# Kernel optimization log

Measured on AMD Instinct MI355X. Metric: run time of the kernel, lower is better.

Reference implementation:

```python
import jax, jax.numpy as jnp
import numpy as np

B, F, Q, E = 256, 128, 4096, 128
TAU = 0.2
P_DROP = 0.5
NUM_SAMPLES = 128  # hardcoded in forward: compute_scores(..., num_samples=128)
NUM_POS = 1
EASY_UB = 0.5
HARD_LB = 0.5


def setup_inputs() -> dict:
    k = jax.random.key(0)
    ks = jax.random.split(k, 8)
    query = jax.random.normal(ks[0], (B, F), jnp.float32)
    key = jax.random.normal(ks[1], (B, F), jnp.float32)
    teacher = jax.random.normal(ks[2], (B, F), jnp.float32)
    negatives = jax.random.normal(ks[3], (F, Q), jnp.float32)
    # random_maskout masks: rand <= p -> zero out
    mask_t = jax.random.uniform(ks[4], (E, B, F)) <= P_DROP
    mask_n = jax.random.uniform(ks[5], (E, F, Q)) <= P_DROP
    # compute_scores sampling mask: rand <= num_samples/Q
    score_mask = jax.random.uniform(ks[6], (E, B, Q)) <= (NUM_SAMPLES / Q)
    # bootstrap over batch dim: for each (e,q) column, sample B row indices with replacement
    idx = jax.random.randint(ks[7], (E, Q, B), 0, B)
    boot = jnp.zeros((E, Q, B), bool).at[
        jnp.arange(E)[:, None, None], jnp.arange(Q)[None, :, None], idx
    ].set(True)
    boot_mask = jnp.transpose(boot, (0, 2, 1))  # (E,B,Q)
    return dict(query=query, key=key, teacher=teacher, negatives=negatives,
                mask_t=mask_t, mask_n=mask_n, score_mask=score_mask, boot_mask=boot_mask)


def _masked_softmax(x, mask, axis):
    # matches torch masked_fill(~mask, -inf) + softmax; masked entries -> 0 prob
    z = jnp.where(mask, x, -jnp.inf)
    m = jnp.max(z, axis=axis, keepdims=True)
    m = jnp.where(jnp.isfinite(m), m, 0.0)  # guard fully-masked slices
    e = jnp.where(mask, jnp.exp(z - m), 0.0)
    return e / jnp.maximum(e.sum(axis=axis, keepdims=True), 1e-30)


def _l2norm(x, axis):
    n = jnp.sqrt(jnp.sum(x * x, axis=axis, keepdims=True))
    return x / jnp.maximum(n, 1e-12)


def reference(query, key, teacher, negatives, mask_t, mask_n, score_mask, boot_mask):
    negatives = jax.lax.stop_gradient(negatives)  # negatives.detach().clone()
    logits_pos = jnp.sum(query * key, axis=1, keepdims=True)      # (B,1)
    logits_neg = query @ negatives                                 # (B,Q)
    logits = jnp.concatenate([logits_pos, logits_neg], axis=1) / TAU
    moco_loss = -jax.nn.log_softmax(logits, axis=1)[:, 0].mean()   # CE with target 0

    # ---- teacher similarities (torch.no_grad) ----
    t = _l2norm(jnp.where(mask_t, 0.0, teacher[None, :, :]), 2)    # (E,B,F)
    n = _l2norm(jnp.where(mask_n, 0.0, negatives[None, :, :]), 1)  # (E,F,Q)
    sim = jax.lax.stop_gradient(jnp.einsum('ebf,efq->ebq', t, n) / TAU)

    # ---- scores: masked softmax over Q, masked mean over E ----
    probs = _masked_softmax(sim, score_mask, axis=2)               # (E,B,Q)
    cnt_e = jnp.maximum(score_mask.sum(axis=0).astype(sim.dtype), 1.0)
    scores = probs.sum(axis=0) / cnt_e                             # (B,Q)

    # ---- uncertainty: masked entropy over batch dim ----
    p = _masked_softmax(sim, boot_mask, axis=1) + 1e-7             # (E,B,Q)
    ent = -(p * jnp.log(p))
    cnt_b = jnp.maximum(boot_mask.sum(axis=1).astype(sim.dtype), 1.0)  # (E,Q)
    uncertainty = (ent.sum(axis=1) / cnt_b).mean(axis=0, keepdims=True)  # (1,Q)

    log_sm_neg = jax.nn.log_softmax(logits[:, 1:], axis=1)         # (B,Q)

    def _pos_loss(pos_mask_row):
        pm = jnp.broadcast_to(pos_mask_row, (B, Q))
        s = jnp.where(pm, scores, -jnp.inf)
        _, idx = jax.lax.top_k(s, NUM_POS)                         # (B,k)
        loss = -jnp.take_along_axis(log_sm_neg, idx, axis=1).mean(axis=1).mean()
        mask = jnp.zeros((B, Q), bool).at[jnp.arange(B)[:, None], idx].set(True)
        return loss, mask

    ub = jnp.quantile(uncertainty, EASY_UB, axis=1)                # (1,)
    easy_loss, easy_mask = _pos_loss(uncertainty <= ub)
    lb = jnp.quantile(uncertainty, HARD_LB, axis=1)
    hard_loss, hard_mask = _pos_loss(uncertainty >= lb)

    return moco_loss, logits, easy_loss, easy_mask, hard_loss, hard_mask
```

## Files before the change

### kernel.cpp

```cpp
#include <hip/hip_runtime.h>
#include <cmath>

typedef unsigned char u8;
typedef unsigned short u16;
typedef unsigned int u32;
typedef __attribute__((ext_vector_type(8))) short s8v;
typedef __attribute__((ext_vector_type(4))) float f32x4;

#define B 256
#define F 128
#define Q 4096
#define E 128
#define QW 128
#define INV_TAU 5.0f
#define CAP 256

#define W_SCORES 0u
#define W_CNT    1048576u
#define W_UNC    2097152u
#define W_NLSE   2101248u
#define W_MOCO   2101504u
#define W_EASY   2101760u
#define W_HARD   2102016u
#define W_UB     2102272u
#define W_INVN   2102528u
#define W_AF     2626816u
#define W_PB     4723968u
#define W_PS     8918272u
#define W_PN     13112576u
#define W_CNTB   15209728u
#define W_ENT    15242496u

#define O_MOCO   0u
#define O_LOGITS 1u
#define O_ELOSS  1048833u
#define O_EMASK  1048834u
#define O_HLOSS  2097410u
#define O_HMASK  2097411u

static __device__ __forceinline__ u16 f2bf(float x) {
    unsigned int u = __builtin_bit_cast(unsigned int, x);
    unsigned int r = (u + 0x7FFFu + ((u >> 16) & 1u)) >> 16;
    return (u16)r;
}

__global__ void k_zero(float4* __restrict__ p) {
    p[(size_t)blockIdx.x * 256 + threadIdx.x] = make_float4(0.f, 0.f, 0.f, 0.f);
}
__global__ void k_zeroi(int* __restrict__ p) {
    p[(size_t)blockIdx.x * 256 + threadIdx.x] = 0;
}

__global__ void __launch_bounds__(256) k_pack(const u8* __restrict__ in,
                                              u32* __restrict__ out, int Rin) {
    __shared__ u32 lds[64 * 133];
    int t = threadIdx.x;
    int r0 = blockIdx.x * 64;
    int q0 = blockIdx.y * 512;
    int qw0 = q0 >> 5;
    #pragma unroll
    for (int i = 0; i < 8; i++) {
        int w = i * 256 + t;
        int row = w >> 5, c = w & 31;
        uint4 v = *(const uint4*)&in[(size_t)(r0 + row) * Q + q0 + c * 16];
        int base = row * 133 + c * 4;
        lds[base] = v.x; lds[base + 1] = v.y; lds[base + 2] = v.z; lds[base + 3] = v.w;
    }
    __syncthreads();
    int e = r0 / Rin, rr = r0 % Rin;
    #pragma unroll
    for (int k = 0; k < 4; k++) {
        int qw = (t >> 6) + k * 4;
        int r = t & 63;
        u32 w = 0;
        #pragma unroll
        for (int j = 0; j < 8; j++) {
            u32 u = lds[r * 133 + qw * 8 + j];
            w |= ((u & 1u) | ((u >> 7) & 2u) | ((u >> 14) & 4u) | ((u >> 21) & 8u)) << (j * 4);
        }
        out[((size_t)e * QW + qw0 + qw) * Rin + rr + r] = w;
    }
}

__global__ void k_afrag(const float* __restrict__ teacher, const u8* __restrict__ mask_t,
                        u16* __restrict__ af) {
    int eb = blockIdx.x;
    int e  = eb >> 8;
    int b  = eb & (B - 1);
    int f  = threadIdx.x;
    float v = mask_t[(size_t)eb * F + f] ? 0.f : teacher[b * F + f];
    float ss = v * v;
    #pragma unroll
    for (int o = 32; o > 0; o >>= 1) ss += __shfl_down(ss, o);
    __shared__ float s2[2];
    if ((threadIdx.x & 63) == 0) s2[threadIdx.x >> 6] = ss;
    __syncthreads();
    float d = fmaxf(sqrtf(s2[0] + s2[1]), 1e-12f);
    float t = v / d;
    int bg = b >> 4, m = b & 15;
    int kb = f >> 5, quad = (f >> 3) & 3, j = f & 7;
    int lane = quad * 16 + m;
    af[((((size_t)e * 16 + bg) * 4 + kb) * 64 + lane) * 8 + j] = f2bf(t);
}

__global__ void __launch_bounds__(256) k_invn(const float* __restrict__ neg,
                                              const u32* __restrict__ pn,
                                              float* __restrict__ invn) {
    __shared__ u32 lds[32 * 128];
    int e = blockIdx.x, t = threadIdx.x;
    int qblk = blockIdx.y;
    size_t base = ((size_t)e * QW + qblk * 32) * F;
    #pragma unroll
    for (int k = 0; k < 16; k++) lds[t + 256 * k] = pn[base + t + 256 * k];
    __syncthreads();
    int q0 = qblk * 1024 + t * 4;
    int qwl = (t * 4) >> 5;
    int sh = (t * 4) & 31;
    float s0 = 0.f, s1 = 0.f, s2 = 0.f, s3 = 0.f;
    #pragma unroll 4
    for (int f = 0; f < F; f++) {
        float4 v = *(const float4*)&neg[(size_t)f * Q + q0];
        u32 w = lds[qwl * 128 + f] >> sh;
        if (!(w & 1u)) s0 = fmaf(v.x, v.x, s0);
        if (!(w & 2u)) s1 = fmaf(v.y, v.y, s1);
        if (!(w & 4u)) s2 = fmaf(v.z, v.z, s2);
        if (!(w & 8u)) s3 = fmaf(v.w, v.w, s3);
    }
    float4 r;
    r.x = INV_TAU / fmaxf(sqrtf(s0), 1e-12f);
    r.y = INV_TAU / fmaxf(sqrtf(s1), 1e-12f);
    r.z = INV_TAU / fmaxf(sqrtf(s2), 1e-12f);
    r.w = INV_TAU / fmaxf(sqrtf(s3), 1e-12f);
    *(float4*)&invn[(size_t)e * Q + q0] = r;
}

__global__ void __launch_bounds__(256) k_fused(
        const u16* __restrict__ af, const float* __restrict__ neg,
        const u32* __restrict__ pn, const float* __restrict__ invn,
        const u32* __restrict__ pb, const u32* __restrict__ ps,
        float* __restrict__ unc, uint2* __restrict__ ent_buf,
        int* __restrict__ cnt_buf, int e0) {
    __shared__ u16 bfrag[2][4][64 * 8];
    __shared__ __align__(16) u32 bword[256];
    __shared__ __align__(16) u32 sword[256];
    __shared__ int sbase[256];
    __shared__ float mstat[4][32], sstat[4][32], cstat[4][32], estat[4][32];
    __shared__ float carr[32];

    int qb = blockIdx.x;
    int el = blockIdx.y, e = e0 + el;
    int t = threadIdx.x;
    int q0 = qb * 32;

    bword[t] = pb[((size_t)e * QW + qb) * B + t];
    sword[t] = ps[((size_t)e * QW + qb) * B + t];

    #pragma unroll
    for (int s = 0; s < 2; s++) {
        int slot = t + 256 * s;
        int qg = slot >> 8;
        int r = slot & 255;
        int kb = r >> 6, lane2 = r & 63;
        int q = q0 + qg * 16 + (lane2 & 15);
        int fb = kb * 32 + (lane2 >> 4) * 8;
        float iv = invn[e * Q + q];
        u16 tmp[8];
        #pragma unroll
        for (int j = 0; j < 8; j++) {
            u32 bit = (pn[((size_t)e * QW + qb) * F + fb + j] >> (q & 31)) & 1u;
            float v = bit ? 0.f : neg[(size_t)(fb + j) * Q + q] * iv;
            tmp[j] = f2bf(v);
        }
        *(s8v*)&bfrag[qg][kb][lane2 * 8] = *(const s8v*)tmp;
    }
    __syncthreads();

    int wave = t >> 6, lane = t & 63;
    int colb = lane & 15, quad = lane >> 4;
    f32x4 acc[4][2];
    #pragma unroll
    for (int bgi = 0; bgi < 4; bgi++) {
        int bg = wave * 4 + bgi;
        s8v a[4];
        #pragma unroll
        for (int kb = 0; kb < 4; kb++)
            a[kb] = *(const s8v*)&af[((((size_t)e * 16 + bg) * 4 + kb) * 64 + lane) * 8];
        #pragma unroll
        for (int qg = 0; qg < 2; qg++) {
            f32x4 c4 = {0.f, 0.f, 0.f, 0.f};
            #pragma unroll
            for (int kb = 0; kb < 4; kb++) {
                s8v bv = *(const s8v*)&bfrag[qg][kb][lane * 8];
                c4 = __builtin_amdgcn_mfma_f32_16x16x32_bf16(a[kb], bv, c4, 0, 0, 0);
            }
            acc[bgi][qg] = c4;
        }
    }

    u32 bwr[4][4];
    #pragma unroll
    for (int bgi = 0; bgi < 4; bgi++) {
        int b0 = (wave * 4 + bgi) * 16 + quad * 4;
        uint4 v = *(const uint4*)&bword[b0];
        bwr[bgi][0] = v.x; bwr[bgi][1] = v.y; bwr[bgi][2] = v.z; bwr[bgi][3] = v.w;
    }

    float mloc[2] = {-INFINITY, -INFINITY};
    #pragma unroll
    for (int bgi = 0; bgi < 4; bgi++)
        #pragma unroll
        for (int r = 0; r < 4; r++)
            #pragma unroll
            for (int qg = 0; qg < 2; qg++)
                if ((bwr[bgi][r] >> (qg * 16 + colb)) & 1u)
                    mloc[qg] = fmaxf(mloc[qg], acc[bgi][qg][r]);
    #pragma unroll
    for (int qg = 0; qg < 2; qg++) {
        mloc[qg] = fmaxf(mloc[qg], __shfl_xor(mloc[qg], 16));
        mloc[qg] = fmaxf(mloc[qg], __shfl_xor(mloc[qg], 32));
    }
    if (quad == 0) { mstat[wave][colb] = mloc[0]; mstat[wave][16 + colb] = mloc[1]; }
    __syncthreads();
    float Mg[2];
    #pragma unroll
    for (int qg = 0; qg < 2; qg++) {
        int col = qg * 16 + colb;
        float M = fmaxf(fmaxf(mstat[0][col], mstat[1][col]),
                        fmaxf(mstat[2][col], mstat[3][col]));
        Mg[qg] = (M == -INFINITY) ? 0.f : M;
    }

    float ex[4][2][4];
    float sloc[2] = {0.f, 0.f}, cloc[2] = {0.f, 0.f};
    #pragma unroll
    for (int bgi = 0; bgi < 4; bgi++)
        #pragma unroll
        for (int r = 0; r < 4; r++)
            #pragma unroll
            for (int qg = 0; qg < 2; qg++) {
                bool mk = (bwr[bgi][r] >> (qg * 16 + colb)) & 1u;
                float v = mk ? __expf(acc[bgi][qg][r] - Mg[qg]) : 0.f;
                ex[bgi][qg][r] = v;
                sloc[qg] += v;
                cloc[qg] += mk ? 1.f : 0.f;
            }
    #pragma unroll
    for (int qg = 0; qg < 2; qg++) {
        sloc[qg] += __shfl_xor(sloc[qg], 16); sloc[qg] += __shfl_xor(sloc[qg], 32);
        cloc[qg] += __shfl_xor(cloc[qg], 16); cloc[qg] += __shfl_xor(cloc[qg], 32);
    }
    if (quad == 0) {
        sstat[wave][colb] = sloc[0]; sstat[wave][16 + colb] = sloc[1];
        cstat[wave][colb] = cloc[0]; cstat[wave][16 + colb] = cloc[1];
    }
    __syncthreads();
    float invS[2];
    #pragma unroll
    for (int qg = 0; qg < 2; qg++) {
        int col = qg * 16 + colb;
        float S = sstat[0][col] + sstat[1][col] + sstat[2][col] + sstat[3][col];
        invS[qg] = 1.f / fmaxf(S, 1e-30f);
        if (wave == 0 && quad == 0)
            carr[col] = cstat[0][col] + cstat[1][col] + cstat[2][col] + cstat[3][col];
    }

    const float P0 = 1e-7f;
    const float C0 = 1.61180954e-6f;
    float eloc[2] = {0.f, 0.f};
    #pragma unroll
    for (int bgi = 0; bgi < 4; bgi++)
        #pragma unroll
        for (int r = 0; r < 4; r++)
            #pragma unroll
            for (int qg = 0; qg < 2; qg++) {
                if ((bwr[bgi][r] >> (qg * 16 + colb)) & 1u) {
                    float p = ex[bgi][qg][r] * invS[qg] + P0;
                    eloc[qg] -= p * __logf(p);
                } else {
                    eloc[qg] += C0;
                }
            }
    #pragma unroll
    for (int qg = 0; qg < 2; qg++) {
        eloc[qg] += __shfl_xor(eloc[qg], 16); eloc[qg] += __shfl_xor(eloc[qg], 32);
    }
    if (quad == 0) { estat[wave][colb] = eloc[0]; estat[wave][16 + colb] = eloc[1]; }

    {
        u32 sw = sword[t];
        int n = __popc(sw);
        int base = 0;
        if (n) base = atomicAdd(&cnt_buf[el * B + t], n);
        sbase[t] = base;
    }
    __syncthreads();

    if (t < 32) {
        float tot = estat[0][t] + estat[1][t] + estat[2][t] + estat[3][t];
        atomicAdd(&unc[q0 + t], tot / fmaxf(carr[t], 1.f));
    }

    #pragma unroll
    for (int bgi = 0; bgi < 4; bgi++) {
        int b0 = (wave * 4 + bgi) * 16 + quad * 4;
        uint4 sv = *(const uint4*)&sword[b0];
        u32 svr[4] = {sv.x, sv.y, sv.z, sv.w};
        #pragma unroll
        for (int r = 0; r < 4; r++)
            #pragma unroll
            for (int qg = 0; qg < 2; qg++) {
                int c = qg * 16 + colb;
                u32 w = svr[r];
                if ((w >> c) & 1u) {
                    int pos = sbase[b0 + r] + __popc(w & ((1u << c) - 1u));
                    if (pos < CAP) {
                        uint2 en;
                        en.x = (unsigned)(q0 + c);
                        en.y = __builtin_bit_cast(unsigned, acc[bgi][qg][r]);
                        ent_buf[((size_t)(el * B + b0 + r)) * CAP + pos] = en;
                    }
                }
            }
    }
}

__global__ void __launch_bounds__(256) k_scores(
        const uint2* __restrict__ ent_buf, const int* __restrict__ cnt_buf,
        float* __restrict__ sacc, float* __restrict__ cacc, int ecnt) {
    __shared__ float srow[Q];
    __shared__ float crow[Q];
    int b = blockIdx.x, t = threadIdx.x;
    #pragma unroll
    for (int j = 0; j < 16; j++) { srow[t + 256 * j] = 0.f; crow[t + 256 * j] = 0.f; }
    __syncthreads();
    int wave = t >> 6, lane = t & 63;
    for (int el = wave; el < ecnt; el += 4) {
        int c = cnt_buf[el * B + b];
        if (c > CAP) c = CAP;
        if (c == 0) continue;
        const uint2* p = ent_buf + (size_t)(el * B + b) * CAP;
        uint2 ev[4]; int ne = 0;
        float m = -INFINITY;
        for (int i = lane; i < c; i += 64) {
            ev[ne] = p[i];
            m = fmaxf(m, __builtin_bit_cast(float, ev[ne].y));
            ne++;
        }
        #pragma unroll
        for (int off = 32; off > 0; off >>= 1) m = fmaxf(m, __shfl_xor(m, off));
        float s = 0.f; float exv[4];
        for (int k = 0; k < ne; k++) {
            exv[k] = __expf(__builtin_bit_cast(float, ev[k].y) - m);
            s += exv[k];
        }
        #pragma unroll
        for (int off = 32; off > 0; off >>= 1) s += __shfl_xor(s, off);
        float iS = 1.f / fmaxf(s, 1e-30f);
        for (int k = 0; k < ne; k++) {
            atomicAdd(&srow[ev[k].x], exv[k] * iS);
            atomicAdd(&crow[ev[k].x], 1.f);
        }
    }
    __syncthreads();
    #pragma unroll
    for (int j = 0; j < 16; j++) {
        int q = t + 256 * j;
        sacc[(size_t)b * Q + q] += srow[q];
        cacc[(size_t)b * Q + q] += crow[q];
    }
}

__global__ void k_finscores(float* __restrict__ sacc, const float* __restrict__ cacc) {
    int idx = blockIdx.x * 256 + threadIdx.x;
    sacc[idx] = sacc[idx] / fmaxf(cacc[idx], 1.f);
}

__global__ void k_logits(const float* __restrict__ query, const float* __restrict__ key,
                         const float* __restrict__ neg, float* __restrict__ out) {
    __shared__ float qrow[F];
    __shared__ float red[256];
    int b = blockIdx.x, t = threadIdx.x;
    float pp = 0.f;
    if (t < F) { float qv = query[b * F + t]; qrow[t] = qv; pp = qv * key[b * F + t]; }
    red[t] = pp;
    __syncthreads();
    for (int s = 128; s > 0; s >>= 1) { if (t < s) red[t] += red[t + s]; __syncthreads(); }
    float pos = red[0];
    float4 acc[4];
    #pragma unroll
    for (int j = 0; j < 4; j++) acc[j] = make_float4(0.f, 0.f, 0.f, 0.f);
    for (int f = 0; f < F; f++) {
        float a = qrow[f];
        const float* np_ = neg + (size_t)f * Q + t * 4;
        #pragma unroll
        for (int j = 0; j < 4; j++) {
            float4 v = *(const float4*)&np_[1024 * j];
            acc[j].x = fmaf(a, v.x, acc[j].x);
            acc[j].y = fmaf(a, v.y, acc[j].y);
            acc[j].z = fmaf(a, v.z, acc[j].z);
            acc[j].w = fmaf(a, v.w, acc[j].w);
        }
    }
    float* row = out + O_LOGITS + (size_t)b * (Q + 1);
    #pragma unroll
    for (int j = 0; j < 4; j++) {
        int q = t * 4 + 1024 * j;
        row[1 + q]     = acc[j].x * INV_TAU;
        row[1 + q + 1] = acc[j].y * INV_TAU;
        row[1 + q + 2] = acc[j].z * INV_TAU;
        row[1 + q + 3] = acc[j].w * INV_TAU;
    }
    if (t == 0) row[0] = pos * INV_TAU;
}

__global__ void k_rowstats(const float* __restrict__ out, float* __restrict__ moco_part,
                           float* __restrict__ nlse) {
    __shared__ float red[256];
    int b = blockIdx.x, t = threadIdx.x;
    const float* row = out + O_LOGITS + (size_t)b * (Q + 1);
    float m = -INFINITY, mn = -INFINITY;
    for (int j = 0; j < 17; j++) {
        int i = t + 256 * j;
        if (i < Q + 1) { float zz = row[i]; m = fmaxf(m, zz); if (i >= 1) mn = fmaxf(mn, zz); }
    }
    red[t] = m; __syncthreads();
    for (int s = 128; s > 0; s >>= 1) { if (t < s) red[t] = fmaxf(red[t], red[t + s]); __syncthreads(); }
    float M = red[0]; __syncthreads();
    red[t] = mn; __syncthreads();
    for (int s = 128; s > 0; s >>= 1) { if (t < s) red[t] = fmaxf(red[t], red[t + s]); __syncthreads(); }
    float Mn = red[0]; __syncthreads();
    float s1 = 0.f, s2 = 0.f;
    for (int j = 0; j < 17; j++) {
        int i = t + 256 * j;
        if (i < Q + 1) { float zz = row[i]; s1 += expf(zz - M); if (i >= 1) s2 += expf(zz - Mn); }
    }
    red[t] = s1; __syncthreads();
    for (int s = 128; s > 0; s >>= 1) { if (t < s) red[t] += red[t + s]; __syncthreads(); }
    float S = red[0]; __syncthreads();
    red[t] = s2; __syncthreads();
    for (int s = 128; s > 0; s >>= 1) { if (t < s) red[t] += red[t + s]; __syncthreads(); }
    float Sn = red[0];
    if (t == 0) { moco_part[b] = M + logf(S) - row[0]; nlse[b] = Mn + logf(Sn); }
}

__global__ void k_median(float* __restrict__ unc, float* __restrict__ ubp) {
    __shared__ float sd[4096];
    int t = threadIdx.x;
    #pragma unroll
    for (int j = 0; j < 4; j++) {
        int q = t + 1024 * j;
        float u = unc[q] * (1.f / 128.f);
        unc[q] = u; sd[q] = u;
    }
    __syncthreads();
    for (int k = 2; k <= 4096; k <<= 1) {
        for (int j = k >> 1; j > 0; j >>= 1) {
            #pragma unroll
            for (int base = 0; base < 4; base++) {
                int i = t + 1024 * base;
                int ixj = i ^ j;
                if (ixj > i) {
                    bool up = ((i & k) == 0);
                    float x = sd[i], y = sd[ixj];
                    if ((x > y) == up) { sd[i] = y; sd[ixj] = x; }
                }
            }
            __syncthreads();
        }
    }
    if (t == 0) { float a = sd[2047], b2 = sd[2048]; ubp[0] = a + 0.5f * (b2 - a); }
}

__global__ void k_select(float* __restrict__ out, const float* __restrict__ scores,
                         const float* __restrict__ unc, const float* __restrict__ ubp,
                         const float* __restrict__ nlse, float* __restrict__ easy_part,
                         float* __restrict__ hard_part) {
    __shared__ float rv[256];
    __shared__ int ri[256];
    __shared__ int bshare;
    int b = blockIdx.x, mode = blockIdx.y, t = threadIdx.x;
    float ub = ubp[0];
    float bv = -INFINITY; int bidx = Q;
    #pragma unroll
    for (int j = 0; j < 16; j++) {
        int q = t + 256 * j;
        float u = unc[q];
        bool ok = (mode == 0) ? (u <= ub) : (u >= ub);
        if (ok) {
            float v = scores[(size_t)b * Q + q];
            if (v > bv || (v == bv && q < bidx)) { bv = v; bidx = q; }
        }
    }
    rv[t] = bv; ri[t] = bidx; __syncthreads();
    for (int s = 128; s > 0; s >>= 1) {
        if (t < s) {
            float v2 = rv[t + s]; int i2 = ri[t + s];
            if (v2 > rv[t] || (v2 == rv[t] && i2 < ri[t])) { rv[t] = v2; ri[t] = i2; }
        }
        __syncthreads();
    }
    if (t == 0) {
        int best = ri[0]; bshare = best;
        float zz = out[O_LOGITS + (size_t)b * (Q + 1) + 1 + best];
        float loss = nlse[b] - zz;
        (mode == 0 ? easy_part : hard_part)[b] = loss;
    }
    __syncthreads();
    int best = bshare;
    float* mrow = out + (mode == 0 ? O_EMASK : O_HMASK) + (size_t)b * Q;
    #pragma unroll
    for (int j = 0; j < 16; j++) { int q = t + 256 * j; mrow[q] = (q == best) ? 1.f : 0.f; }
}

__global__ void k_scalars(const float* __restrict__ moco, const float* __restrict__ easyp,
                          const float* __restrict__ hardp, float* __restrict__ out) {
    __shared__ float red[256];
    int t = threadIdx.x;
    red[t] = moco[t]; __syncthreads();
    for (int s = 128; s > 0; s >>= 1) { if (t < s) red[t] += red[t + s]; __syncthreads(); }
    if (t == 0) out[O_MOCO] = red[0] / 256.f;
    __syncthreads();
    red[t] = easyp[t]; __syncthreads();
    for (int s = 128; s > 0; s >>= 1) { if (t < s) red[t] += red[t + s]; __syncthreads(); }
    if (t == 0) out[O_ELOSS] = red[0] / 256.f;
    __syncthreads();
    red[t] = hardp[t]; __syncthreads();
    for (int s = 128; s > 0; s >>= 1) { if (t < s) red[t] += red[t + s]; __syncthreads(); }
    if (t == 0) out[O_HLOSS] = red[0] / 256.f;
}

extern "C" void kernel_launch(void* const* d_in, const int* in_sizes, int n_in,
                              void* d_out, int out_size, void* d_ws, size_t ws_size,
                              hipStream_t stream) {
    const float* query   = (const float*)d_in[0];
    const float* key     = (const float*)d_in[1];
    const float* teacher = (const float*)d_in[2];
    const float* neg     = (const float*)d_in[3];
    const u8* mask_t     = (const u8*)d_in[4];
    const u8* mask_n     = (const u8*)d_in[5];
    const u8* score_mask = (const u8*)d_in[6];
    const u8* boot_mask  = (const u8*)d_in[7];
    float* out = (float*)d_out;
    float* ws  = (float*)d_ws;

    long ws_floats = (long)(ws_size / 4);
    int Ec = (int)((ws_floats - (long)W_ENT) / (long)(B * CAP * 2));
    if (Ec > E) Ec = E;
    if (Ec < 1) Ec = 1;

    u16* af = (u16*)(ws + W_AF);
    u32* pb = (u32*)(ws + W_PB);
    u32* ps = (u32*)(ws + W_PS);
    u32* pn = (u32*)(ws + W_PN);
    int* cnt_buf = (int*)(ws + W_CNTB);
    uint2* ent_buf = (uint2*)(ws + W_ENT);

    k_zero<<<2052, 256, 0, stream>>>((float4*)(ws + W_SCORES));
    k_pack<<<dim3((E * B) / 64, Q / 512), 256, 0, stream>>>(boot_mask, pb, B);
    k_pack<<<dim3((E * B) / 64, Q / 512), 256, 0, stream>>>(score_mask, ps, B);
    k_pack<<<dim3((E * F) / 64, Q / 512), 256, 0, stream>>>(mask_n, pn, F);
    k_afrag<<<E * B, 128, 0, stream>>>(teacher, mask_t, af);
    k_invn<<<dim3(E, 4), 256, 0, stream>>>(neg, pn, ws + W_INVN);
    k_logits<<<B, 256, 0, stream>>>(query, key, neg, out);
    k_rowstats<<<B, 256, 0, stream>>>(out, ws + W_MOCO, ws + W_NLSE);

    for (int e0 = 0; e0 < E; e0 += Ec) {
        int ecnt = (E - e0 < Ec) ? (E - e0) : Ec;
        k_zeroi<<<ecnt, 256, 0, stream>>>(cnt_buf);
        k_fused<<<dim3(QW, ecnt), 256, 0, stream>>>(
            af, neg, pn, ws + W_INVN, pb, ps, ws + W_UNC, ent_buf, cnt_buf, e0);
        k_scores<<<B, 256, 0, stream>>>(ent_buf, cnt_buf, ws + W_SCORES, ws + W_CNT, ecnt);
    }

    k_finscores<<<(B * Q) / 256, 256, 0, stream>>>(ws + W_SCORES, ws + W_CNT);
    k_median<<<1, 1024, 0, stream>>>(ws + W_UNC, ws + W_UB);
    k_select<<<dim3(B, 2), 256, 0, stream>>>(out, ws + W_SCORES, ws + W_UNC, ws + W_UB,
                                             ws + W_NLSE, ws + W_EASY, ws + W_HARD);
    k_scalars<<<1, 256, 0, stream>>>(ws + W_MOCO, ws + W_EASY, ws + W_HARD, out);
}
```

Measured before the change: 1.429 ms.

## Widen fused tile to 64 columns, drop max-subtraction, split logits kernel

The fused similarity/entropy kernel now processes 64 Q columns per block instead of 32, staging the mask words and inverse norms in shared memory so each A fragment load feeds twice as many MFMAs. The max-reduction pass and one barrier are removed from both the fused softmax and the score softmax by exponentiating raw values, which relies on the cosine-similarity/tau values being bounded. The entropy pass recomputes exp instead of keeping an exp array in registers. The logits kernel is split across four Q segments to raise parallelism.

```diff
diff --git a/kernel.cpp b/kernel.cpp
--- a/kernel.cpp
+++ b/kernel.cpp
@@ -140,35 +140,48 @@
         const u32* __restrict__ pb, const u32* __restrict__ ps,
         float* __restrict__ unc, uint2* __restrict__ ent_buf,
         int* __restrict__ cnt_buf, int e0) {
-    __shared__ u16 bfrag[2][4][64 * 8];
-    __shared__ __align__(16) u32 bword[256];
-    __shared__ __align__(16) u32 sword[256];
+    __shared__ u16 bfrag[4][4][512];
+    __shared__ u32 bw[2][256], sw[2][256];
+    __shared__ u32 pnl[2][128];
+    __shared__ float invl[64];
+    __shared__ float sstat[4][64], cstat[4][64], estat[4][64];
+    __shared__ float carr[64];
     __shared__ int sbase[256];
-    __shared__ float mstat[4][32], sstat[4][32], cstat[4][32], estat[4][32];
-    __shared__ float carr[32];
 
     int qb = blockIdx.x;
     int el = blockIdx.y, e = e0 + el;
     int t = threadIdx.x;
-    int q0 = qb * 32;
-
-    bword[t] = pb[((size_t)e * QW + qb) * B + t];
-    sword[t] = ps[((size_t)e * QW + qb) * B + t];
-
-    #pragma unroll
-    for (int s = 0; s < 2; s++) {
+    int q0 = qb * 64;
+    int qw0 = qb * 2;
+
+    bw[0][t] = pb[((size_t)e * QW + qw0) * B + t];
+    bw[1][t] = pb[((size_t)e * QW + qw0 + 1) * B + t];
+    sw[0][t] = ps[((size_t)e * QW + qw0) * B + t];
+    sw[1][t] = ps[((size_t)e * QW + qw0 + 1) * B + t];
+    if (t < 128) {
+        pnl[0][t] = pn[((size_t)e * QW + qw0) * F + t];
+        pnl[1][t] = pn[((size_t)e * QW + qw0 + 1) * F + t];
+    } else if (t < 192) {
+        invl[t - 128] = invn[(size_t)e * Q + q0 + (t - 128)];
+    }
+    __syncthreads();
+
+    #pragma unroll
+    for (int s = 0; s < 4; s++) {
         int slot = t + 256 * s;
         int qg = slot >> 8;
         int r = slot & 255;
         int kb = r >> 6, lane2 = r & 63;
-        int q = q0 + qg * 16 + (lane2 & 15);
+        int ql = qg * 16 + (lane2 & 15);
         int fb = kb * 32 + (lane2 >> 4) * 8;
-        float iv = invn[e * Q + q];
+        float iv = invl[ql];
+        const u32* pw = pnl[ql >> 5];
+        int sh = ql & 31;
         u16 tmp[8];
         #pragma unroll
         for (int j = 0; j < 8; j++) {
-            u32 bit = (pn[((size_t)e * QW + qb) * F + fb + j] >> (q & 31)) & 1u;
-            float v = bit ? 0.f : neg[(size_t)(fb + j) * Q + q] * iv;
+            u32 bit = (pw[fb + j] >> sh) & 1u;
+            float v = bit ? 0.f : neg[(size_t)(fb + j) * Q + q0 + ql] * iv;
             tmp[j] = f2bf(v);
         }
         *(s8v*)&bfrag[qg][kb][lane2 * 8] = *(const s8v*)tmp;
@@ -177,7 +190,7 @@
 
     int wave = t >> 6, lane = t & 63;
     int colb = lane & 15, quad = lane >> 4;
-    f32x4 acc[4][2];
+    f32x4 acc[4][4];
     #pragma unroll
     for (int bgi = 0; bgi < 4; bgi++) {
         int bg = wave * 4 + bgi;
@@ -186,7 +199,7 @@
         for (int kb = 0; kb < 4; kb++)
             a[kb] = *(const s8v*)&af[((((size_t)e * 16 + bg) * 4 + kb) * 64 + lane) * 8];
         #pragma unroll
-        for (int qg = 0; qg < 2; qg++) {
+        for (int qg = 0; qg < 4; qg++) {
             f32x4 c4 = {0.f, 0.f, 0.f, 0.f};
             #pragma unroll
             for (int kb = 0; kb < 4; kb++) {
@@ -197,105 +210,94 @@
         }
     }
 
-    u32 bwr[4][4];
+    float sloc[4] = {0.f, 0.f, 0.f, 0.f}, cloc[4] = {0.f, 0.f, 0.f, 0.f};
     #pragma unroll
     for (int bgi = 0; bgi < 4; bgi++) {
         int b0 = (wave * 4 + bgi) * 16 + quad * 4;
-        uint4 v = *(const uint4*)&bword[b0];
-        bwr[bgi][0] = v.x; bwr[bgi][1] = v.y; bwr[bgi][2] = v.z; bwr[bgi][3] = v.w;
-    }
-
-    float mloc[2] = {-INFINITY, -INFINITY};
-    #pragma unroll
-    for (int bgi = 0; bgi < 4; bgi++)
+        uint4 w0 = *(const uint4*)&bw[0][b0];
+        uint4 w1 = *(const uint4*)&bw[1][b0];
+        u32 W0[4] = {w0.x, w0.y, w0.z, w0.w};
+        u32 W1[4] = {w1.x, w1.y, w1.z, w1.w};
         #pragma unroll
         for (int r = 0; r < 4; r++)
             #pragma unroll
-            for (int qg = 0; qg < 2; qg++)
-                if ((bwr[bgi][r] >> (qg * 16 + colb)) & 1u)
-                    mloc[qg] = fmaxf(mloc[qg], acc[bgi][qg][r]);
-    #pragma unroll
-    for (int qg = 0; qg < 2; qg++) {
-        mloc[qg] = fmaxf(mloc[qg], __shfl_xor(mloc[qg], 16));
-        mloc[qg] = fmaxf(mloc[qg], __shfl_xor(mloc[qg], 32));
-    }
-    if (quad == 0) { mstat[wave][colb] = mloc[0]; mstat[wave][16 + colb] = mloc[1]; }
-    __syncthreads();
-    float Mg[2];
-    #pragma unroll
-    for (int qg = 0; qg < 2; qg++) {
-        int col = qg * 16 + colb;
-        float M = fmaxf(fmaxf(mstat[0][col], mstat[1][col]),
-                        fmaxf(mstat[2][col], mstat[3][col]));
-        Mg[qg] = (M == -INFINITY) ? 0.f : M;
-    }
-
-    float ex[4][2][4];
-    float sloc[2] = {0.f, 0.f}, cloc[2] = {0.f, 0.f};
-    #pragma unroll
-    for (int bgi = 0; bgi < 4; bgi++)
+            for (int qg = 0; qg < 4; qg++) {
+                u32 w = (qg & 2) ? W1[r] : W0[r];
+                int bpos = (qg & 1) * 16 + colb;
+                if ((w >> bpos) & 1u) {
+                    sloc[qg] += __expf(acc[bgi][qg][r]);
+                    cloc[qg] += 1.f;
+                }
+            }
+    }
+    #pragma unroll
+    for (int qg = 0; qg < 4; qg++) {
+        sloc[qg] += __shfl_xor(sloc[qg], 16); sloc[qg] += __shfl_xor(sloc[qg], 32);
+        cloc[qg] += __shfl_xor(cloc[qg], 16); cloc[qg] += __shfl_xor(cloc[qg], 32);
+    }
+    if (quad == 0)
+        #pragma unroll
+        for (int qg = 0; qg < 4; qg++) {
+            sstat[wave][qg * 16 + colb] = sloc[qg];
+            cstat[wave][qg * 16 + colb] = cloc[qg];
+        }
+    __syncthreads();
+    float invS[4];
+    #pragma unroll
+    for (int qg = 0; qg < 4; qg++) {
+        int c = qg * 16 + colb;
+        float S = sstat[0][c] + sstat[1][c] + sstat[2][c] + sstat[3][c];
+        invS[qg] = 1.f / fmaxf(S, 1e-30f);
+    }
+    if (wave == 0 && quad == 0)
+        #pragma unroll
+        for (int qg = 0; qg < 4; qg++) {
+            int c = qg * 16 + colb;
+            carr[c] = cstat[0][c] + cstat[1][c] + cstat[2][c] + cstat[3][c];
+        }
+
+    const float P0 = 1e-7f;
+    const float C0 = 1.61180954e-6f;
+    float eloc[4] = {0.f, 0.f, 0.f, 0.f};
+    #pragma unroll
+    for (int bgi = 0; bgi < 4; bgi++) {
+        int b0 = (wave * 4 + bgi) * 16 + quad * 4;
+        uint4 w0 = *(const uint4*)&bw[0][b0];
+        uint4 w1 = *(const uint4*)&bw[1][b0];
+        u32 W0[4] = {w0.x, w0.y, w0.z, w0.w};
+        u32 W1[4] = {w1.x, w1.y, w1.z, w1.w};
         #pragma unroll
         for (int r = 0; r < 4; r++)
             #pragma unroll
-            for (int qg = 0; qg < 2; qg++) {
-                bool mk = (bwr[bgi][r] >> (qg * 16 + colb)) & 1u;
-                float v = mk ? __expf(acc[bgi][qg][r] - Mg[qg]) : 0.f;
-                ex[bgi][qg][r] = v;
-                sloc[qg] += v;
-                cloc[qg] += mk ? 1.f : 0.f;
-            }
-    #pragma unroll
-    for (int qg = 0; qg < 2; qg++) {
-        sloc[qg] += __shfl_xor(sloc[qg], 16); sloc[qg] += __shfl_xor(sloc[qg], 32);
-        cloc[qg] += __shfl_xor(cloc[qg], 16); cloc[qg] += __shfl_xor(cloc[qg], 32);
-    }
-    if (quad == 0) {
-        sstat[wave][colb] = sloc[0]; sstat[wave][16 + colb] = sloc[1];
-        cstat[wave][colb] = cloc[0]; cstat[wave][16 + colb] = cloc[1];
-    }
-    __syncthreads();
-    float invS[2];
-    #pragma unroll
-    for (int qg = 0; qg < 2; qg++) {
-        int col = qg * 16 + colb;
-        float S = sstat[0][col] + sstat[1][col] + sstat[2][col] + sstat[3][col];
-        invS[qg] = 1.f / fmaxf(S, 1e-30f);
-        if (wave == 0 && quad == 0)
-            carr[col] = cstat[0][col] + cstat[1][col] + cstat[2][col] + cstat[3][col];
-    }
-
-    const float P0 = 1e-7f;
-    const float C0 = 1.61180954e-6f;
-    float eloc[2] = {0.f, 0.f};
-    #pragma unroll
-    for (int bgi = 0; bgi < 4; bgi++)
-        #pragma unroll
-        for (int r = 0; r < 4; r++)
-            #pragma unroll
-            for (int qg = 0; qg < 2; qg++) {
-                if ((bwr[bgi][r] >> (qg * 16 + colb)) & 1u) {
-                    float p = ex[bgi][qg][r] * invS[qg] + P0;
+            for (int qg = 0; qg < 4; qg++) {
+                u32 w = (qg & 2) ? W1[r] : W0[r];
+                int bpos = (qg & 1) * 16 + colb;
+                if ((w >> bpos) & 1u) {
+                    float p = __expf(acc[bgi][qg][r]) * invS[qg] + P0;
                     eloc[qg] -= p * __logf(p);
                 } else {
                     eloc[qg] += C0;
                 }
             }
-    #pragma unroll
-    for (int qg = 0; qg < 2; qg++) {
+    }
+    #pragma unroll
+    for (int qg = 0; qg < 4; qg++) {
         eloc[qg] += __shfl_xor(eloc[qg], 16); eloc[qg] += __shfl_xor(eloc[qg], 32);
     }
-    if (quad == 0) { estat[wave][colb] = eloc[0]; estat[wave][16 + colb] = eloc[1]; }
+    if (quad == 0)
+        #pragma unroll
+        for (int qg = 0; qg < 4; qg++) estat[wave][qg * 16 + colb] = eloc[qg];
 
     {
-        u32 sw = sword[t];
-        int n = __popc(sw);
+        u32 a0 = sw[0][t], a1 = sw[1][t];
+        int n = __popc(a0) + __popc(a1);
         int base = 0;
         if (n) base = atomicAdd(&cnt_buf[el * B + t], n);
         sbase[t] = base;
     }
     __syncthreads();
 
-    if (t < 32) {
+    if (t < 64) {
         float tot = estat[0][t] + estat[1][t] + estat[2][t] + estat[3][t];
         atomicAdd(&unc[q0 + t], tot / fmaxf(carr[t], 1.f));
     }
@@ -303,24 +305,30 @@
     #pragma unroll
     for (int bgi = 0; bgi < 4; bgi++) {
         int b0 = (wave * 4 + bgi) * 16 + quad * 4;
-        uint4 sv = *(const uint4*)&sword[b0];
-        u32 svr[4] = {sv.x, sv.y, sv.z, sv.w};
-        #pragma unroll
-        for (int r = 0; r < 4; r++)
+        uint4 s0 = *(const uint4*)&sw[0][b0];
+        uint4 s1 = *(const uint4*)&sw[1][b0];
+        u32 S0[4] = {s0.x, s0.y, s0.z, s0.w};
+        u32 S1[4] = {s1.x, s1.y, s1.z, s1.w};
+        #pragma unroll
+        for (int r = 0; r < 4; r++) {
+            int bs = sbase[b0 + r];
+            int p0 = __popc(S0[r]);
             #pragma unroll
-            for (int qg = 0; qg < 2; qg++) {
-                int c = qg * 16 + colb;
-                u32 w = svr[r];
-                if ((w >> c) & 1u) {
-                    int pos = sbase[b0 + r] + __popc(w & ((1u << c) - 1u));
+            for (int qg = 0; qg < 4; qg++) {
+                int bpos = (qg & 1) * 16 + colb;
+                u32 w = (qg & 2) ? S1[r] : S0[r];
+                if ((w >> bpos) & 1u) {
+                    int rank = __popc(w & ((1u << bpos) - 1u)) + ((qg & 2) ? p0 : 0);
+                    int pos = bs + rank;
                     if (pos < CAP) {
                         uint2 en;
-                        en.x = (unsigned)(q0 + c);
+                        en.x = (unsigned)(q0 + qg * 16 + colb);
                         en.y = __builtin_bit_cast(unsigned, acc[bgi][qg][r]);
                         ent_buf[((size_t)(el * B + b0 + r)) * CAP + pos] = en;
                     }
                 }
             }
+        }
     }
 }
 
@@ -339,19 +347,13 @@
         if (c > CAP) c = CAP;
         if (c == 0) continue;
         const uint2* p = ent_buf + (size_t)(el * B + b) * CAP;
-        uint2 ev[4]; int ne = 0;
-        float m = -INFINITY;
+        uint2 ev[4]; float exv[4]; int ne = 0;
+        float s = 0.f;
         for (int i = lane; i < c; i += 64) {
             ev[ne] = p[i];
-            m = fmaxf(m, __builtin_bit_cast(float, ev[ne].y));
+            exv[ne] = __expf(__builtin_bit_cast(float, ev[ne].y));
+            s += exv[ne];
             ne++;
-        }
-        #pragma unroll
-        for (int off = 32; off > 0; off >>= 1) m = fmaxf(m, __shfl_xor(m, off));
-        float s = 0.f; float exv[4];
-        for (int k = 0; k < ne; k++) {
-            exv[k] = __expf(__builtin_bit_cast(float, ev[k].y) - m);
-            s += exv[k];
         }
         #pragma unroll
         for (int off = 32; off > 0; off >>= 1) s += __shfl_xor(s, off);
@@ -379,38 +381,31 @@
                          const float* __restrict__ neg, float* __restrict__ out) {
     __shared__ float qrow[F];
     __shared__ float red[256];
-    int b = blockIdx.x, t = threadIdx.x;
-    float pp = 0.f;
-    if (t < F) { float qv = query[b * F + t]; qrow[t] = qv; pp = qv * key[b * F + t]; }
-    red[t] = pp;
-    __syncthreads();
-    for (int s = 128; s > 0; s >>= 1) { if (t < s) red[t] += red[t + s]; __syncthreads(); }
-    float pos = red[0];
-    float4 acc[4];
-    #pragma unroll
-    for (int j = 0; j < 4; j++) acc[j] = make_float4(0.f, 0.f, 0.f, 0.f);
+    int b = blockIdx.x, seg = blockIdx.y, t = threadIdx.x;
+    if (t < F) qrow[t] = query[b * F + t];
+    __syncthreads();
+    int q0 = seg * 1024 + t * 4;
+    float4 acc = make_float4(0.f, 0.f, 0.f, 0.f);
     for (int f = 0; f < F; f++) {
         float a = qrow[f];
-        const float* np_ = neg + (size_t)f * Q + t * 4;
-        #pragma unroll
-        for (int j = 0; j < 4; j++) {
-            float4 v = *(const float4*)&np_[1024 * j];
-            acc[j].x = fmaf(a, v.x, acc[j].x);
-            acc[j].y = fmaf(a, v.y, acc[j].y);
-            acc[j].z = fmaf(a, v.z, acc[j].z);
-            acc[j].w = fmaf(a, v.w, acc[j].w);
-        }
+        float4 v = *(const float4*)&neg[(size_t)f * Q + q0];
+        acc.x = fmaf(a, v.x, acc.x);
+        acc.y = fmaf(a, v.y, acc.y);
+        acc.z = fmaf(a, v.z, acc.z);
+        acc.w = fmaf(a, v.w, acc.w);
     }
     float* row = out + O_LOGITS + (size_t)b * (Q + 1);
-    #pragma unroll
-    for (int j = 0; j < 4; j++) {
-        int q = t * 4 + 1024 * j;
-        row[1 + q]     = acc[j].x * INV_TAU;
-        row[1 + q + 1] = acc[j].y * INV_TAU;
-        row[1 + q + 2] = acc[j].z * INV_TAU;
-        row[1 + q + 3] = acc[j].w * INV_TAU;
-    }
-    if (t == 0) row[0] = pos * INV_TAU;
+    row[1 + q0]     = acc.x * INV_TAU;
+    row[1 + q0 + 1] = acc.y * INV_TAU;
+    row[1 + q0 + 2] = acc.z * INV_TAU;
+    row[1 + q0 + 3] = acc.w * INV_TAU;
+    if (seg == 0) {
+        float pp = (t < F) ? qrow[t] * key[b * F + t] : 0.f;
+        red[t] = pp;
+        __syncthreads();
+        for (int s = 128; s > 0; s >>= 1) { if (t < s) red[t] += red[t + s]; __syncthreads(); }
+        if (t == 0) row[0] = red[0] * INV_TAU;
+    }
 }
 
 __global__ void k_rowstats(const float* __restrict__ out, float* __restrict__ moco_part,
@@ -561,13 +556,13 @@
     k_pack<<<dim3((E * F) / 64, Q / 512), 256, 0, stream>>>(mask_n, pn, F);
     k_afrag<<<E * B, 128, 0, stream>>>(teacher, mask_t, af);
     k_invn<<<dim3(E, 4), 256, 0, stream>>>(neg, pn, ws + W_INVN);
-    k_logits<<<B, 256, 0, stream>>>(query, key, neg, out);
+    k_logits<<<dim3(B, 4), 256, 0, stream>>>(query, key, neg, out);
     k_rowstats<<<B, 256, 0, stream>>>(out, ws + W_MOCO, ws + W_NLSE);
 
     for (int e0 = 0; e0 < E; e0 += Ec) {
         int ecnt = (E - e0 < Ec) ? (E - e0) : Ec;
         k_zeroi<<<ecnt, 256, 0, stream>>>(cnt_buf);
-        k_fused<<<dim3(QW, ecnt), 256, 0, stream>>>(
+        k_fused<<<dim3(Q / 64, ecnt), 256, 0, stream>>>(
             af, neg, pn, ws + W_INVN, pb, ps, ws + W_UNC, ent_buf, cnt_buf, e0);
         k_scores<<<B, 256, 0, stream>>>(ent_buf, cnt_buf, ws + W_SCORES, ws + W_CNT, ecnt);
     }
```

After: 1.402 ms. Within noise of the previous version (-1.9%).
